# Kernel optimization log

Measured on AMD Instinct MI355X. Metric: run time of the kernel, lower is better.

The kernel has to match this reference:

```python
import jax, jax.numpy as jnp
import numpy as np

EPS = 1e-6
NUM_HEADS = 12


def _layernorm(x, eps=EPS):
    m = jnp.mean(x, axis=-1, keepdims=True)
    v = jnp.var(x, axis=-1, keepdims=True)
    return (x - m) * jax.lax.rsqrt(v + eps)


def _rmsnorm(x, w, eps=EPS):
    ms = jnp.mean(jnp.square(x), axis=-1, keepdims=True)
    return x * jax.lax.rsqrt(ms + eps) * w


def _rope_interleaved(x, cos, sin):
    # x: [B, L, H, hd]; cos/sin: [L, hd//2]; is_neox_style=False (interleaved pairs)
    x1 = x[..., 0::2]
    x2 = x[..., 1::2]
    c = cos[None, :, None, :]
    s = sin[None, :, None, :]
    o1 = x1 * c - x2 * s
    o2 = x1 * s + x2 * c
    return jnp.stack([o1, o2], axis=-1).reshape(x.shape)


def _attention(q, k, v, mask=None):
    # q: [B, Lq, H, hd], k/v: [B, Lk, H, hd]
    hd = q.shape[-1]
    scale = 1.0 / jnp.sqrt(jnp.asarray(hd, q.dtype))
    scores = jnp.einsum('blhd,bmhd->bhlm', q, k) * scale
    if mask is not None:
        scores = jnp.where(mask[None, None], scores, jnp.finfo(scores.dtype).min)
    p = jax.nn.softmax(scores, axis=-1)
    return jnp.einsum('bhlm,bmhd->blhd', p, v)


def setup_inputs() -> dict:
    key = jax.random.key(0)
    B, F, FS, D, FF, LC = 1, 2, 1560, 1536, 8960, 512
    L = F * FS
    hd = D // NUM_HEADS
    ks = jax.random.split(key, 32)
    i = iter(range(32))
    n = lambda shape, s=0.02: jax.random.normal(ks[next(i)], shape, jnp.float32) * s
    inp = {
        'hidden_states': n((B, L, D), 1.0),
        'encoder_hidden_states': n((B, LC, D), 1.0),
        'temb': n((B, F, 6, D), 1.0),
    }
    pos = jnp.arange(L, dtype=jnp.float32)
    inv = 1.0 / (10000.0 ** (jnp.arange(hd // 2, dtype=jnp.float32) / (hd // 2)))
    ang = pos[:, None] * inv[None, :]
    inp['cos'] = jnp.cos(ang)
    inp['sin'] = jnp.sin(ang)
    fidx = jnp.arange(L) // FS
    inp['attn_mask'] = fidx[:, None] >= fidx[None, :]  # frame-level block-causal
    # params
    inp['sst'] = n((1, 6, D), 1.0 / np.sqrt(D))
    for name in ['wq', 'wk', 'wv', 'wo']:
        inp[name] = n((D, D))
    for name in ['bq', 'bk', 'bv', 'bo']:
        inp[name] = jnp.zeros((D,), jnp.float32)
    inp['nq_w'] = jnp.ones((D,), jnp.float32)
    inp['nk_w'] = jnp.ones((D,), jnp.float32)
    inp['ln2_g'] = jnp.ones((D,), jnp.float32)
    inp['ln2_b'] = jnp.zeros((D,), jnp.float32)
    for name in ['cwq', 'cwk', 'cwv', 'cwo']:
        inp[name] = n((D, D))
    for name in ['cbq', 'cbk', 'cbv', 'cbo']:
        inp[name] = jnp.zeros((D,), jnp.float32)
    inp['cnq_w'] = jnp.ones((D,), jnp.float32)
    inp['cnk_w'] = jnp.ones((D,), jnp.float32)
    inp['w1'] = n((D, FF))
    inp['b1'] = jnp.zeros((FF,), jnp.float32)
    inp['w2'] = n((FF, D))
    inp['b2'] = jnp.zeros((D,), jnp.float32)
    return inp


def reference(hidden_states, encoder_hidden_states, temb, cos, sin, attn_mask,
              sst, wq, bq, wk, bk, wv, bv, wo, bo, nq_w, nk_w, ln2_g, ln2_b,
              cwq, cbq, cwk, cbk, cwv, cbv, cwo, cbo, cnq_w, cnk_w,
              w1, b1, w2, b2):
    B, L, D = hidden_states.shape
    F = temb.shape[1]
    FS = L // F
    H = NUM_HEADS
    hd = D // H

    e = sst[:, None] + temb  # [B, F, 6, D]
    shift_msa, scale_msa, gate_msa = e[:, :, 0], e[:, :, 1], e[:, :, 2]
    c_shift, c_scale, c_gate = e[:, :, 3], e[:, :, 4], e[:, :, 5]

    # --- self attention ---
    nh = _layernorm(hidden_states).reshape(B, F, FS, D)
    nh = (nh * (1.0 + scale_msa[:, :, None]) + shift_msa[:, :, None]).reshape(B, L, D)
    q = _rmsnorm(nh @ wq + bq, nq_w).reshape(B, L, H, hd)
    k = _rmsnorm(nh @ wk + bk, nk_w).reshape(B, L, H, hd)
    v = (nh @ wv + bv).reshape(B, L, H, hd)
    q = _rope_interleaved(q, cos, sin)
    k = _rope_interleaved(k, cos, sin)
    attn_out = _attention(q, k, v, attn_mask).reshape(B, L, D) @ wo + bo

    h = hidden_states + (attn_out.reshape(B, F, FS, D) * gate_msa[:, :, None]).reshape(B, L, D)
    norm_h = _layernorm(h) * ln2_g + ln2_b  # null shift/scale

    # --- cross attention ---
    LC = encoder_hidden_states.shape[1]
    cq = _rmsnorm(norm_h @ cwq + cbq, cnq_w).reshape(B, L, H, hd)
    ck = _rmsnorm(encoder_hidden_states @ cwk + cbk, cnk_w).reshape(B, LC, H, hd)
    cv = (encoder_hidden_states @ cwv + cbv).reshape(B, LC, H, hd)
    cross_out = _attention(cq, ck, cv).reshape(B, L, D) @ cwo + cbo

    h = h + cross_out  # gate = 1
    norm_h = _layernorm(h).reshape(B, F, FS, D)
    norm_h = (norm_h * (1.0 + c_scale[:, :, None]) + c_shift[:, :, None]).reshape(B, L, D)

    # --- ffn ---
    ff = jax.nn.gelu(norm_h @ w1 + b1, approximate=True) @ w2 + b2
    h = h + (ff.reshape(B, F, FS, D) * c_gate[:, :, None]).reshape(B, L, D)
    return h
```

## Files before the change

kernel.cpp:

```cpp
#include <hip/hip_runtime.h>
#include <hip/hip_bf16.h>
#include <math.h>

typedef __bf16 bf16;
typedef __bf16 bf16x8 __attribute__((ext_vector_type(8)));
typedef float  f32x4  __attribute__((ext_vector_type(4)));
typedef unsigned int u32;

#define DMODEL 1536
#define NHEADS 12
#define HD 128
#define HDH 64

__device__ __forceinline__ void async16(const void* g, void* l) {
  __builtin_amdgcn_global_load_lds((const __attribute__((address_space(1))) u32*)g,
                                   (__attribute__((address_space(3))) u32*)l, 16, 0, 0);
}

__device__ inline void block_reduce2(float& a, float& b) {
  __shared__ float sa[4], sb[4];
  #pragma unroll
  for (int off = 32; off; off >>= 1) {
    a += __shfl_xor(a, off);
    b += __shfl_xor(b, off);
  }
  int w = threadIdx.x >> 6;
  if ((threadIdx.x & 63) == 0) { sa[w] = a; sb[w] = b; }
  __syncthreads();
  a = sa[0] + sa[1] + sa[2] + sa[3];
  b = sb[0] + sb[1] + sb[2] + sb[3];
  __syncthreads();
}

__global__ __launch_bounds__(256)
void ln_kernel(const float* __restrict__ X, bf16* __restrict__ Y,
               const float* __restrict__ sst, const float* __restrict__ temb,
               const float* __restrict__ g, const float* __restrict__ bvec,
               int jshift, int jscale, int FS, int mode)
{
  int row = blockIdx.x;
  const float* x = X + (size_t)row * DMODEL;
  float v[6];
  float s1 = 0.f, s2 = 0.f;
  #pragma unroll
  for (int i = 0; i < 6; i++) {
    float t = x[threadIdx.x + i * 256];
    v[i] = t; s1 += t; s2 += t * t;
  }
  block_reduce2(s1, s2);
  float mean = s1 * (1.f / DMODEL);
  float var  = s2 * (1.f / DMODEL) - mean * mean;
  float rs = rsqrtf(var + 1e-6f);
  int f = row / FS;
  bf16* y = Y + (size_t)row * DMODEL;
  #pragma unroll
  for (int i = 0; i < 6; i++) {
    int d = threadIdx.x + i * 256;
    float t = (v[i] - mean) * rs;
    float o;
    if (mode == 0) {
      float sc = sst[jscale * DMODEL + d] + temb[(f * 6 + jscale) * DMODEL + d];
      float sh = sst[jshift * DMODEL + d] + temb[(f * 6 + jshift) * DMODEL + d];
      o = t * (1.f + sc) + sh;
    } else {
      o = t * g[d] + bvec[d];
    }
    y[d] = (bf16)o;
  }
}

__global__ __launch_bounds__(256)
void rms_rope_kernel(const float* __restrict__ P, int S, long long MN,
                     const bf16* __restrict__ Xb, int RS, int CO,
                     const float* __restrict__ bias, bf16* __restrict__ Y,
                     const float* __restrict__ w,
                     const float* __restrict__ cosb, const float* __restrict__ sinb,
                     int dorope, float oscale)
{
  __shared__ float rowbuf[DMODEL];
  int row = blockIdx.x;
  float v[6];
  float s2 = 0.f, dummy = 0.f;
  if (Xb) {
    const bf16* x = Xb + (size_t)row * RS + CO;
    #pragma unroll
    for (int i = 0; i < 6; i++) {
      int d = threadIdx.x + i * 256;
      float t = (float)x[d];
      v[i] = t; rowbuf[d] = t; s2 += t * t;
    }
  } else {
    const float* x = P + (size_t)row * RS + CO;
    #pragma unroll
    for (int i = 0; i < 6; i++) {
      int d = threadIdx.x + i * 256;
      float t = bias[d];
      for (int s = 0; s < S; s++) t += x[(size_t)s * MN + d];
      v[i] = t; rowbuf[d] = t; s2 += t * t;
    }
  }
  __syncthreads();
  block_reduce2(s2, dummy);
  float rs = rsqrtf(s2 * (1.f / DMODEL) + 1e-6f) * oscale;
  bf16* y = Y + (size_t)row * DMODEL;
  if (dorope) {
    #pragma unroll
    for (int i = 0; i < 3; i++) {
      int p = threadIdx.x + i * 256;
      int d0 = 2 * p, d1 = 2 * p + 1;
      float y0 = rowbuf[d0] * rs * w[d0];
      float y1 = rowbuf[d1] * rs * w[d1];
      int ih = p & 63;
      float c = cosb[(size_t)row * HDH + ih];
      float s = sinb[(size_t)row * HDH + ih];
      y[d0] = (bf16)(y0 * c - y1 * s);
      y[d1] = (bf16)(y0 * s + y1 * c);
    }
  } else {
    #pragma unroll
    for (int i = 0; i < 6; i++) {
      int d = threadIdx.x + i * 256;
      y[d] = (bf16)(v[i] * rs * w[d]);
    }
  }
}

__global__ __launch_bounds__(256)
void wt_kernel(const float* __restrict__ W, bf16* __restrict__ Wt, int K, int N)
{
  __shared__ float T[32][33];
  int k0 = blockIdx.x * 32, n0 = blockIdx.y * 32;
  int tx = threadIdx.x & 31, ty = threadIdx.x >> 5;
  #pragma unroll
  for (int i = 0; i < 4; i++)
    T[ty + 8 * i][tx] = W[(size_t)(k0 + ty + 8 * i) * N + n0 + tx];
  __syncthreads();
  #pragma unroll
  for (int i = 0; i < 4; i++)
    Wt[(size_t)(n0 + ty + 8 * i) * K + k0 + tx] = (bf16)T[tx][ty + 8 * i];
}

__global__ __launch_bounds__(256)
void catbias_kernel(float* __restrict__ bqkv, const float* __restrict__ bq,
                    const float* __restrict__ bk, const float* __restrict__ bv,
                    float* __restrict__ cbkv, const float* __restrict__ cbk,
                    const float* __restrict__ cbv)
{
  int i = blockIdx.x * 256 + threadIdx.x;
  if (i < DMODEL) {
    bqkv[i] = bq[i]; bqkv[DMODEL + i] = bk[i]; bqkv[2 * DMODEL + i] = bv[i];
    cbkv[i] = cbk[i]; cbkv[DMODEL + i] = cbv[i];
  }
}

__global__ __launch_bounds__(256)
void gemm_bt(const bf16* __restrict__ A, const bf16* __restrict__ Bt,
             const float* __restrict__ bias, float* __restrict__ Cf,
             bf16* __restrict__ Cb, int M, int N, int K, int act,
             int Ks, long long MN)
{
  __shared__ bf16 As[128 * 32];
  __shared__ bf16 Bs[128 * 32];
  int tid = threadIdx.x, lane = tid & 63, w = tid >> 6;
  int wm = w >> 1, wn = w & 1;
  int l16 = lane & 15, quad = lane >> 4;

  int gx = (M + 127) >> 7, gy = N >> 7;
  int per_panel = gx << 3;
  int bid = blockIdx.x;
  int panel = bid / per_panel;
  int rem = bid - panel * per_panel;
  int pc0 = panel << 3;
  int ncols = gy - pc0; if (ncols > 8) ncols = 8;
  int by = pc0 + rem % ncols;
  int bx = rem / ncols;
  int bm = bx * 128, bn = by * 128;

  int kb0 = blockIdx.y * Ks;

  int rl = lane >> 2;
  int kk = (lane & 3) * 8;
  int r0 = (2 * w) * 16 + rl, r1 = (2 * w + 1) * 16 + rl;
  int am0 = bm + r0; if (am0 > M - 1) am0 = M - 1;
  int am1 = bm + r1; if (am1 > M - 1) am1 = M - 1;
  const bf16* a0 = A + (size_t)am0 * K + kk;
  const bf16* a1 = A + (size_t)am1 * K + kk;
  const bf16* b0 = Bt + (size_t)(bn + r0) * K + kk;
  const bf16* b1 = Bt + (size_t)(bn + r1) * K + kk;
  bf16* lA0 = As + (2 * w) * 512; bf16* lA1 = As + (2 * w + 1) * 512;
  bf16* lB0 = Bs + (2 * w) * 512; bf16* lB1 = Bs + (2 * w + 1) * 512;

  f32x4 acc[4][4] = {};
  int kend = kb0 + Ks;
  for (int k0 = kb0; k0 < kend; k0 += 32) {
    async16(a0 + k0, lA0);
    async16(a1 + k0, lA1);
    async16(b0 + k0, lB0);
    async16(b1 + k0, lB1);
    __syncthreads();
    bf16x8 af[4], bfv[4];
    #pragma unroll
    for (int mi = 0; mi < 4; mi++)
      af[mi] = *(const bf16x8*)&As[(wm * 64 + mi * 16 + l16) * 32 + quad * 8];
    #pragma unroll
    for (int ni = 0; ni < 4; ni++)
      bfv[ni] = *(const bf16x8*)&Bs[(wn * 64 + ni * 16 + l16) * 32 + quad * 8];
    #pragma unroll
    for (int mi = 0; mi < 4; mi++)
      #pragma unroll
      for (int ni = 0; ni < 4; ni++)
        acc[mi][ni] = __builtin_amdgcn_mfma_f32_16x16x32_bf16(af[mi], bfv[ni], acc[mi][ni], 0, 0, 0);
    __syncthreads();
  }
  float* Cfo = Cf ? Cf + (size_t)blockIdx.y * MN : nullptr;
  #pragma unroll
  for (int mi = 0; mi < 4; mi++) {
    #pragma unroll
    for (int r = 0; r < 4; r++) {
      int m = bm + wm * 64 + mi * 16 + quad * 4 + r;
      if (m < M) {
        #pragma unroll
        for (int ni = 0; ni < 4; ni++) {
          int n = bn + wn * 64 + ni * 16 + l16;
          float val = acc[mi][ni][r] + (bias ? bias[n] : 0.f);
          if (act == 1) {
            float u = val + 0.044715f * val * val * val;
            float z = 1.5957691216057308f * u;
            val = val / (1.f + __expf(-z));
          }
          if (Cfo) Cfo[(size_t)m * N + n] = val;
          else     Cb[(size_t)m * N + n] = (bf16)val;
        }
      }
    }
  }
}

__global__ __launch_bounds__(512, 2)
void gemm256(const bf16* __restrict__ A, const bf16* __restrict__ Bt,
             const float* __restrict__ bias, float* __restrict__ Cf,
             bf16* __restrict__ Cb, int M, int N, int K, int act,
             int Ks, long long MN)
{
  __shared__ bf16 LDS[2][2][128 * 128];
  int tid = threadIdx.x, lane = tid & 63, w = tid >> 6;
  int wm = w >> 2, wn = w & 3;
  int l16 = lane & 15, quad = lane >> 4;

  int gmx = (M + 255) >> 8;
  int bx = blockIdx.x % gmx, by = blockIdx.x / gmx;
  int bm = bx << 8, bn = by << 8;
  int kb0 = blockIdx.y * Ks;
  int NT = Ks >> 6;

  int aro = (l16 * 64 + quad * 16) ^ ((l16 >> 3) << 5);
  const char* A0r = (const char*)&LDS[0][0][0] + wm * 16384 + aro;
  const char* A1r = (const char*)&LDS[1][0][0] + wm * 16384 + aro;
  const char* B0r = (const char*)&LDS[0][1][0] + wn * 8192 + aro;
  const char* B1r = (const char*)&LDS[1][1][0] + wn * 8192 + aro;

  int srl = lane >> 2;
  int sc16 = (lane & 3) ^ (((lane >> 5) & 1) << 1);
  int Mm1 = M - 1, Nm1 = N - 1;
  int ga0 = bm + w * 16 + srl;        if (ga0 > Mm1) ga0 = Mm1;
  int ga1 = bm + 128 + w * 16 + srl;  if (ga1 > Mm1) ga1 = Mm1;
  int gb0 = bn + w * 16 + srl;        if (gb0 > Nm1) gb0 = Nm1;
  int gb1 = bn + 128 + w * 16 + srl;  if (gb1 > Nm1) gb1 = Nm1;
  const bf16* Ag0 = A + (size_t)ga0 * K + sc16 * 8;
  const bf16* Ag1 = A + (size_t)ga1 * K + sc16 * 8;
  const bf16* Bg0 = Bt + (size_t)gb0 * K + sc16 * 8;
  const bf16* Bg1 = Bt + (size_t)gb1 * K + sc16 * 8;
  char* wA0[2] = { (char*)&LDS[0][0][0] + w * 2048, (char*)&LDS[1][0][0] + w * 2048 };
  char* wA1[2] = { wA0[0] + 16384, wA0[1] + 16384 };
  char* wB0[2] = { (char*)&LDS[0][1][0] + w * 2048, (char*)&LDS[1][1][0] + w * 2048 };
  char* wB1[2] = { wB0[0] + 16384, wB0[1] + 16384 };

#define STG(src, kk_, dst) do { const bf16* _s = (src) + (kk_); \
    async16(_s, (dst)); async16(_s + 32, (dst) + 1024); } while (0)
#define MFMA_(d, a, b) d = __builtin_amdgcn_mfma_f32_16x16x32_bf16(a, b, d, 0, 0, 0)

  STG(Ag0, kb0, wA0[0]); STG(Ag1, kb0, wA1[0]);
  STG(Bg0, kb0, wB0[0]); STG(Bg1, kb0, wB1[0]);
  if (NT > 1) {
    STG(Bg0, kb0 + 64, wB0[1]); STG(Bg1, kb0 + 64, wB1[1]);
    asm volatile("s_waitcnt vmcnt(4)" ::: "memory");
  } else {
    asm volatile("s_waitcnt vmcnt(0)" ::: "memory");
  }
  __builtin_amdgcn_s_barrier();

  f32x4 acc[8][4] = {};
  for (int t = 0; t < NT; ++t) {
    int b = t & 1;
    const char* Ab = b ? A1r : A0r;
    const char* Bb = b ? B1r : B0r;
    int kt1 = kb0 + (t + 1) * 64;
    int kt2 = kt1 + 64;
    bool st1 = (t + 1) < NT, st2 = (t + 2) < NT;

    bf16x8 a0[8], b0v[4];
    #pragma unroll
    for (int i = 0; i < 8; i++) a0[i] = *(const bf16x8*)(Ab + i * 1024);
    #pragma unroll
    for (int i = 0; i < 4; i++) b0v[i] = *(const bf16x8*)(Bb + i * 1024);
    if (st1) STG(Ag0, kt1, wA0[b ^ 1]);
    __builtin_amdgcn_s_barrier();
    asm volatile("s_waitcnt lgkmcnt(0)" ::: "memory");
    __builtin_amdgcn_s_setprio(1);
    #pragma unroll
    for (int mi = 0; mi < 4; mi++)
      #pragma unroll
      for (int ni = 0; ni < 2; ni++) {
        MFMA_(acc[mi][ni], a0[mi * 2],     b0v[ni * 2]);
        MFMA_(acc[mi][ni], a0[mi * 2 + 1], b0v[ni * 2 + 1]);
      }
    __builtin_amdgcn_s_setprio(0);
    __builtin_amdgcn_s_barrier();

    bf16x8 b1v[4];
    #pragma unroll
    for (int i = 0; i < 4; i++) b1v[i] = *(const bf16x8*)(Bb + (4 + i) * 1024);
    if (st1) STG(Ag1, kt1, wA1[b ^ 1]);
    __builtin_amdgcn_s_barrier();
    asm volatile("s_waitcnt lgkmcnt(0)" ::: "memory");
    __builtin_amdgcn_s_setprio(1);
    #pragma unroll
    for (int mi = 0; mi < 4; mi++)
      #pragma unroll
      for (int ni = 0; ni < 2; ni++) {
        MFMA_(acc[mi][2 + ni], a0[mi * 2],     b1v[ni * 2]);
        MFMA_(acc[mi][2 + ni], a0[mi * 2 + 1], b1v[ni * 2 + 1]);
      }
    __builtin_amdgcn_s_setprio(0);
    __builtin_amdgcn_s_barrier();

    bf16x8 a1[8];
    #pragma unroll
    for (int i = 0; i < 8; i++) a1[i] = *(const bf16x8*)(Ab + (8 + i) * 1024);
    if (st2) STG(Bg0, kt2, wB0[b]);
    __builtin_amdgcn_s_barrier();
    asm volatile("s_waitcnt lgkmcnt(0)" ::: "memory");
    __builtin_amdgcn_s_setprio(1);
    #pragma unroll
    for (int mi = 0; mi < 4; mi++)
      #pragma unroll
      for (int ni = 0; ni < 2; ni++) {
        MFMA_(acc[4 + mi][2 + ni], a1[mi * 2],     b1v[ni * 2]);
        MFMA_(acc[4 + mi][2 + ni], a1[mi * 2 + 1], b1v[ni * 2 + 1]);
      }
    __builtin_amdgcn_s_setprio(0);
    __builtin_amdgcn_s_barrier();

    if (st2) STG(Bg1, kt2, wB1[b]);
    __builtin_amdgcn_s_setprio(1);
    #pragma unroll
    for (int mi = 0; mi < 4; mi++)
      #pragma unroll
      for (int ni = 0; ni < 2; ni++) {
        MFMA_(acc[4 + mi][ni], a1[mi * 2],     b0v[ni * 2]);
        MFMA_(acc[4 + mi][ni], a1[mi * 2 + 1], b0v[ni * 2 + 1]);
      }
    __builtin_amdgcn_s_setprio(0);
    if (st2)      { asm volatile("s_waitcnt vmcnt(4)" ::: "memory"); }
    else if (st1) { asm volatile("s_waitcnt vmcnt(0)" ::: "memory"); }
    __builtin_amdgcn_s_barrier();
  }
#undef STG
#undef MFMA_

  float* Cfo = Cf ? Cf + (size_t)blockIdx.y * MN : nullptr;
  #pragma unroll
  for (int mi = 0; mi < 8; mi++) {
    #pragma unroll
    for (int r = 0; r < 4; r++) {
      int m = bm + wm * 128 + mi * 16 + quad * 4 + r;
      if (m < M) {
        #pragma unroll
        for (int ni = 0; ni < 4; ni++) {
          int n = bn + wn * 64 + ni * 16 + l16;
          float val = acc[mi][ni][r] + (bias ? bias[n] : 0.f);
          if (act == 1) {
            float u = val + 0.044715f * val * val * val;
            float z = 1.5957691216057308f * u;
            val = val / (1.f + __expf(-z));
          }
          if (Cfo) Cfo[(size_t)m * N + n] = val;
          else     Cb[(size_t)m * N + n] = (bf16)val;
        }
      }
    }
  }
}

__global__ __launch_bounds__(256)
void transposev_kernel(const bf16* __restrict__ Xb, int RS, int CO,
                       bf16* __restrict__ Vt, int L)
{
  __shared__ bf16 T[64][65];
  int l0 = blockIdx.x * 64, n0 = blockIdx.y * 64;
  int tid = threadIdx.x;
  int r = tid >> 2;
  int c8 = (tid & 3) * 16;
  int lc = l0 + r; if (lc > L - 1) lc = L - 1;
  const bf16* src = Xb + (size_t)lc * RS + CO + n0 + c8;
  #pragma unroll
  for (int i = 0; i < 16; i++) T[r][c8 + i] = src[i];
  __syncthreads();
  #pragma unroll
  for (int i = 0; i < 16; i++) {
    int l = l0 + c8 + i;
    if (l < L) Vt[(size_t)(n0 + r) * L + l] = T[c8 + i][r];
  }
}

__global__ __launch_bounds__(256)
void flash2_kernel(const bf16* __restrict__ Q, const bf16* __restrict__ Kg,
                   const bf16* __restrict__ Vt, bf16* __restrict__ O,
                   int Lq, int Lk, int FS, int causal, int nqb)
{
  __shared__ bf16 Kt[64 * 128];
  __shared__ bf16 Vtile[128 * 64];
  __shared__ bf16 Pl[4][16][72];
  int tid = threadIdx.x, lane = tid & 63, w = tid >> 6;
  int l16 = lane & 15, quad = lane >> 4;
  int bid = blockIdx.x;
  int h = bid % NHEADS;
  int qb = nqb - 1 - (bid / NHEADS);
  int q0b = qb * 64;
  int q0w = q0b + w * 16;

  int qrow = q0w + l16; if (qrow > Lq - 1) qrow = Lq - 1;
  const bf16* qbase = Q + (size_t)qrow * DMODEL + h * HD + quad * 8;
  bf16x8 qf[4];
  #pragma unroll
  for (int dc = 0; dc < 4; dc++) qf[dc] = *(const bf16x8*)(qbase + dc * 32);

  int kvrow[4];
  int kvmin_w = Lk, kv_end = Lk;
  if (causal) {
    #pragma unroll
    for (int r = 0; r < 4; r++) {
      int qr = q0w + quad * 4 + r; if (qr > Lq - 1) qr = Lq - 1;
      kvrow[r] = (qr / FS + 1) * FS;
    }
    int q0c = q0w; if (q0c > Lq - 1) q0c = Lq - 1;
    kvmin_w = (q0c / FS + 1) * FS;
    int qlast = q0b + 63; if (qlast > Lq - 1) qlast = Lq - 1;
    kv_end = (qlast / FS + 1) * FS;
    if (kv_end > Lk) kv_end = Lk;
  }

  f32x4 acc_o[8] = {};
  float m_i[4], l_i[4];
  #pragma unroll
  for (int r = 0; r < 4; r++) { m_i[r] = -1e30f; l_i[r] = 0.f; }

  for (int kb = 0; kb < kv_end; kb += 64) {
    #pragma unroll
    for (int j = 0; j < 4; j++) {
      int u = w * 256 + j * 64 + lane;
      int row = u >> 4;
      int c = (u & 15) ^ (row & 15);
      int krow = kb + row; if (krow > Lk - 1) krow = Lk - 1;
      async16(Kg + (size_t)krow * DMODEL + h * HD + c * 8,
              Kt + (size_t)(w * 256 + j * 64) * 8);
    }
    #pragma unroll
    for (int j = 0; j < 4; j++) {
      int u = w * 256 + j * 64 + lane;
      int row = u >> 3;
      int c = (u & 7) ^ (row & 7);
      async16(Vt + (size_t)(h * HD + row) * Lk + kb + c * 8,
              Vtile + (size_t)(w * 256 + j * 64) * 8);
    }
    __syncthreads();

    f32x4 s[4] = {};
    #pragma unroll
    for (int nk = 0; nk < 4; nk++) {
      #pragma unroll
      for (int dc = 0; dc < 4; dc++) {
        bf16x8 kf = *(const bf16x8*)&Kt[(((nk * 16 + l16) << 4) + ((4 * dc + quad) ^ l16)) * 8];
        s[nk] = __builtin_amdgcn_mfma_f32_16x16x32_bf16(qf[dc], kf, s[nk], 0, 0, 0);
      }
    }

    bool need_mask = causal && (kb + 64 > kvmin_w);
    float p[4][4];
    #pragma unroll
    for (int r = 0; r < 4; r++) {
      #pragma unroll
      for (int nk = 0; nk < 4; nk++) {
        float sv = s[nk][r];
        if (need_mask && (kb + nk * 16 + l16 >= kvrow[r])) sv = -1e30f;
        p[nk][r] = sv;
      }
      float bm = fmaxf(fmaxf(p[0][r], p[1][r]), fmaxf(p[2][r], p[3][r]));
      #pragma unroll
      for (int off = 8; off; off >>= 1) bm = fmaxf(bm, __shfl_xor(bm, off));
      float mn = fmaxf(m_i[r], bm);
      float alpha = __expf(m_i[r] - mn);
      m_i[r] = mn;
      float ps = 0.f;
      #pragma unroll
      for (int nk = 0; nk < 4; nk++) {
        float e = __expf(p[nk][r] - mn);
        p[nk][r] = e; ps += e;
      }
      #pragma unroll
      for (int off = 8; off; off >>= 1) ps += __shfl_xor(ps, off);
      l_i[r] = l_i[r] * alpha + ps;
      #pragma unroll
      for (int t = 0; t < 8; t++) acc_o[t][r] *= alpha;
    }

    #pragma unroll
    for (int nk = 0; nk < 4; nk++)
      #pragma unroll
      for (int r = 0; r < 4; r++)
        Pl[w][quad * 4 + r][nk * 16 + l16] = (bf16)p[nk][r];
    __threadfence_block();
    bf16x8 pf0 = *(const bf16x8*)&Pl[w][l16][quad * 8];
    bf16x8 pf1 = *(const bf16x8*)&Pl[w][l16][32 + quad * 8];

    #pragma unroll
    for (int t = 0; t < 8; t++) {
      bf16x8 vf0 = *(const bf16x8*)&Vtile[(((t * 16 + l16) << 3) + ((quad) ^ (l16 & 7))) * 8];
      bf16x8 vf1 = *(const bf16x8*)&Vtile[(((t * 16 + l16) << 3) + ((4 + quad) ^ (l16 & 7))) * 8];
      acc_o[t] = __builtin_amdgcn_mfma_f32_16x16x32_bf16(pf0, vf0, acc_o[t], 0, 0, 0);
      acc_o[t] = __builtin_amdgcn_mfma_f32_16x16x32_bf16(pf1, vf1, acc_o[t], 0, 0, 0);
    }
    __syncthreads();
  }

  #pragma unroll
  for (int r = 0; r < 4; r++) {
    int m = q0w + quad * 4 + r;
    if (m < Lq) {
      float inv = 1.f / l_i[r];
      bf16* obase = O + (size_t)m * DMODEL + h * HD;
      #pragma unroll
      for (int t = 0; t < 8; t++)
        obase[t * 16 + l16] = (bf16)(acc_o[t][r] * inv);
    }
  }
}

__global__ __launch_bounds__(256)
void modresid_kernel(const float* __restrict__ base, const float* __restrict__ P,
                     int S, long long MN, const float* __restrict__ bias,
                     float* __restrict__ out,
                     const float* __restrict__ sst, const float* __restrict__ temb,
                     int jg, int FS, long long total)
{
  long long i = (long long)blockIdx.x * 256 + threadIdx.x;
  if (i >= total) return;
  int d = (int)(i % DMODEL);
  int f = (int)((i / DMODEL) / FS);
  float g = sst[jg * DMODEL + d] + temb[(f * 6 + jg) * DMODEL + d];
  float v = bias[d];
  for (int s = 0; s < S; s++) v += P[(size_t)s * MN + i];
  out[i] = base[i] + v * g;
}

__global__ __launch_bounds__(256)
void addf_kernel(float* __restrict__ h, const float* __restrict__ P,
                 int S, long long MN, const float* __restrict__ bias, long long total)
{
  long long i = (long long)blockIdx.x * 256 + threadIdx.x;
  if (i >= total) return;
  int d = (int)(i % DMODEL);
  float v = bias[d];
  for (int s = 0; s < S; s++) v += P[(size_t)s * MN + i];
  h[i] += v;
}

__global__ __launch_bounds__(256)
void cast_kernel(const float* __restrict__ x, bf16* __restrict__ y, long long total)
{
  long long i = (long long)blockIdx.x * 256 + threadIdx.x;
  if (i < total) y[i] = (bf16)x[i];
}

extern "C" void kernel_launch(void* const* d_in, const int* in_sizes, int n_in,
                              void* d_out, int out_size, void* d_ws, size_t ws_size,
                              hipStream_t stream)
{
  const float* hs   = (const float*)d_in[0];
  const float* enc  = (const float*)d_in[1];
  const float* temb = (const float*)d_in[2];
  const float* cosb = (const float*)d_in[3];
  const float* sinb = (const float*)d_in[4];
  const float* sst  = (const float*)d_in[6];
  const float* wq = (const float*)d_in[7];
  const float* wk = (const float*)d_in[8];
  const float* wv = (const float*)d_in[9];
  const float* wo = (const float*)d_in[10];
  const float* bq = (const float*)d_in[11];
  const float* bk = (const float*)d_in[12];
  const float* bv = (const float*)d_in[13];
  const float* bo = (const float*)d_in[14];
  const float* nq_w = (const float*)d_in[15];
  const float* nk_w = (const float*)d_in[16];
  const float* ln2_g = (const float*)d_in[17];
  const float* ln2_b = (const float*)d_in[18];
  const float* cwq = (const float*)d_in[19];
  const float* cwk = (const float*)d_in[20];
  const float* cwv = (const float*)d_in[21];
  const float* cwo = (const float*)d_in[22];
  const float* cbq = (const float*)d_in[23];
  const float* cbk = (const float*)d_in[24];
  const float* cbv = (const float*)d_in[25];
  const float* cbo = (const float*)d_in[26];
  const float* cnq_w = (const float*)d_in[27];
  const float* cnk_w = (const float*)d_in[28];
  const float* w1 = (const float*)d_in[29];
  const float* b1 = (const float*)d_in[30];
  const float* w2 = (const float*)d_in[31];
  const float* b2 = (const float*)d_in[32];

  int L  = in_sizes[0] / DMODEL;
  int LC = in_sizes[1] / DMODEL;
  int F  = in_sizes[2] / (6 * DMODEL);
  int FS = L / F;
  int FF = in_sizes[30];
  long long LD = (long long)L * DMODEL;
  float* outp = (float*)d_out;
  int N3 = 3 * DMODEL, N2 = 2 * DMODEL;

  char* p = (char*)d_ws;
  auto alloc = [&](size_t bytes) -> char* {
    char* r = p; p += (bytes + 255) & ~(size_t)255; return r;
  };
  size_t DD = (size_t)DMODEL * DMODEL;
  bf16* wqkv_t = (bf16*)alloc(DD * 3 * 2);
  bf16* wto_t  = (bf16*)alloc(DD * 2);
  bf16* cwq_t  = (bf16*)alloc(DD * 2);
  bf16* cwkv_t = (bf16*)alloc(DD * 2 * 2);
  bf16* cwo_t  = (bf16*)alloc(DD * 2);
  bf16* w1t = (bf16*)alloc((size_t)DMODEL * FF * 2);
  bf16* w2t = (bf16*)alloc((size_t)DMODEL * FF * 2);
  float* bqkv = (float*)alloc((size_t)N3 * 4);
  float* cbkv = (float*)alloc((size_t)N2 * 4);
  float* hbuf = (float*)alloc((size_t)LD * 4);
  bf16* nh   = (bf16*)alloc((size_t)LD * 2);
  bf16* qb   = (bf16*)alloc((size_t)LD * 2);
  bf16* kb   = (bf16*)alloc((size_t)LD * 2);
  bf16* ab   = (bf16*)alloc((size_t)LD * 2);
  bf16* vtc  = (bf16*)alloc((size_t)LC * DMODEL * 2);
  bf16* encb = (bf16*)alloc((size_t)LC * DMODEL * 2);
  char* BIG1 = alloc((size_t)L * FF * 2);
  bf16* qkvb = (bf16*)BIG1;
  bf16* ckvb = (bf16*)BIG1;
  bf16* ffb  = (bf16*)BIG1;
  char* BIG2 = alloc((size_t)LD * 2 * 4);
  bf16* vtb = (bf16*)BIG2;
  float* Pp = (float*)BIG2;
  (void)ws_size; (void)n_in; (void)out_size;

  dim3 gWdd(DMODEL / 32, DMODEL / 32);
  wt_kernel<<<gWdd, 256, 0, stream>>>(wq, wqkv_t, DMODEL, DMODEL);
  wt_kernel<<<gWdd, 256, 0, stream>>>(wk, wqkv_t + DD, DMODEL, DMODEL);
  wt_kernel<<<gWdd, 256, 0, stream>>>(wv, wqkv_t + 2 * DD, DMODEL, DMODEL);
  wt_kernel<<<gWdd, 256, 0, stream>>>(wo, wto_t, DMODEL, DMODEL);
  wt_kernel<<<gWdd, 256, 0, stream>>>(cwq, cwq_t, DMODEL, DMODEL);
  wt_kernel<<<gWdd, 256, 0, stream>>>(cwk, cwkv_t, DMODEL, DMODEL);
  wt_kernel<<<gWdd, 256, 0, stream>>>(cwv, cwkv_t + DD, DMODEL, DMODEL);
  wt_kernel<<<gWdd, 256, 0, stream>>>(cwo, cwo_t, DMODEL, DMODEL);
  wt_kernel<<<dim3(DMODEL / 32, FF / 32), 256, 0, stream>>>(w1, w1t, DMODEL, FF);
  wt_kernel<<<dim3(FF / 32, DMODEL / 32), 256, 0, stream>>>(w2, w2t, FF, DMODEL);
  catbias_kernel<<<6, 256, 0, stream>>>(bqkv, bq, bk, bv, cbkv, cbk, cbv);

  int gxC = (LC + 127) / 128;
  int gmx = (L + 255) / 256;
  int ewg = (int)((LD + 255) / 256);
  int nqb = (L + 63) / 64;
  const float qs = 0.08838834764831845f;

  ln_kernel<<<L, 256, 0, stream>>>(hs, nh, sst, temb, nullptr, nullptr, 0, 1, FS, 0);
  gemm256<<<dim3(gmx * (N3 / 256), 1), 512, 0, stream>>>(nh, wqkv_t, bqkv, nullptr, qkvb,
                                                         L, N3, DMODEL, 0, DMODEL, 0);
  rms_rope_kernel<<<L, 256, 0, stream>>>(nullptr, 0, 0, qkvb, N3, 0, nullptr, qb, nq_w, cosb, sinb, 1, qs);
  rms_rope_kernel<<<L, 256, 0, stream>>>(nullptr, 0, 0, qkvb, N3, DMODEL, nullptr, kb, nk_w, cosb, sinb, 1, 1.0f);
  transposev_kernel<<<dim3((L + 63) / 64, DMODEL / 64), 256, 0, stream>>>(qkvb, N3, 2 * DMODEL, vtb, L);
  flash2_kernel<<<NHEADS * nqb, 256, 0, stream>>>(qb, kb, vtb, ab, L, L, FS, 1, nqb);
  gemm256<<<dim3(gmx * (DMODEL / 256), 2), 512, 0, stream>>>(ab, wto_t, nullptr, Pp, nullptr,
                                                             L, DMODEL, DMODEL, 0, DMODEL / 2, LD);
  modresid_kernel<<<ewg, 256, 0, stream>>>(hs, Pp, 2, LD, bo, hbuf, sst, temb, 2, FS, LD);
  ln_kernel<<<L, 256, 0, stream>>>(hbuf, nh, nullptr, nullptr, ln2_g, ln2_b, 0, 0, FS, 1);
  gemm256<<<dim3(gmx * (DMODEL / 256), 2), 512, 0, stream>>>(nh, cwq_t, nullptr, Pp, nullptr,
                                                             L, DMODEL, DMODEL, 0, DMODEL / 2, LD);
  rms_rope_kernel<<<L, 256, 0, stream>>>(Pp, 2, LD, nullptr, DMODEL, 0, cbq, qb, cnq_w, nullptr, nullptr, 0, qs);
  cast_kernel<<<(int)(((long long)LC * DMODEL + 255) / 256), 256, 0, stream>>>(enc, encb, (long long)LC * DMODEL);
  gemm_bt<<<dim3(gxC * (N2 / 128), 1), 256, 0, stream>>>(encb, cwkv_t, cbkv, nullptr, ckvb,
                                                         LC, N2, DMODEL, 0, DMODEL, 0);
  rms_rope_kernel<<<LC, 256, 0, stream>>>(nullptr, 0, 0, ckvb, N2, 0, nullptr, kb, cnk_w, nullptr, nullptr, 0, 1.0f);
  transposev_kernel<<<dim3((LC + 63) / 64, DMODEL / 64), 256, 0, stream>>>(ckvb, N2, DMODEL, vtc, LC);
  flash2_kernel<<<NHEADS * nqb, 256, 0, stream>>>(qb, kb, vtc, ab, L, LC, FS, 0, nqb);
  gemm256<<<dim3(gmx * (DMODEL / 256), 2), 512, 0, stream>>>(ab, cwo_t, nullptr, Pp, nullptr,
                                                             L, DMODEL, DMODEL, 0, DMODEL / 2, LD);
  addf_kernel<<<ewg, 256, 0, stream>>>(hbuf, Pp, 2, LD, cbo, LD);
  ln_kernel<<<L, 256, 0, stream>>>(hbuf, nh, sst, temb, nullptr, nullptr, 3, 4, FS, 0);
  gemm256<<<dim3(gmx * (FF / 256), 1), 512, 0, stream>>>(nh, w1t, b1, nullptr, ffb,
                                                         L, FF, DMODEL, 1, DMODEL, 0);
  gemm256<<<dim3(gmx * (DMODEL / 256), 2), 512, 0, stream>>>(ffb, w2t, nullptr, Pp, nullptr,
                                                             L, DMODEL, FF, 0, FF / 2, LD);
  modresid_kernel<<<ewg, 256, 0, stream>>>(hbuf, Pp, 2, LD, b2, outp, sst, temb, 5, FS, LD);
}
```

Baseline: 1.157 ms.

## Use grouped panel tile ordering and three-way uneven split-K in GEMMs

Tile indices in gemm256 now follow a panel order: runs of up to eight N-tiles are walked across all M-tiles, so concurrent blocks share B columns for better L2 reuse. Split-K now takes a split count and divides the 64-wide K tiles unevenly, allowing three splits even when K/64 does not divide evenly. The DMODEL-output GEMMs move from 2 to 3 splits to fill more CUs on a 12x6 tile grid. The cost is more fp32 partial-sum traffic and a larger workspace, which the reduction kernels now read as three partials.

```diff
diff --git a/kernel.cpp b/kernel.cpp
--- a/kernel.cpp
+++ b/kernel.cpp
@@ -240,18 +240,30 @@
 void gemm256(const bf16* __restrict__ A, const bf16* __restrict__ Bt,
              const float* __restrict__ bias, float* __restrict__ Cf,
              bf16* __restrict__ Cb, int M, int N, int K, int act,
-             int Ks, long long MN)
+             int S, long long MN)
 {
   __shared__ bf16 LDS[2][2][128 * 128];
   int tid = threadIdx.x, lane = tid & 63, w = tid >> 6;
   int wm = w >> 2, wn = w & 3;
   int l16 = lane & 15, quad = lane >> 4;
 
-  int gmx = (M + 255) >> 8;
-  int bx = blockIdx.x % gmx, by = blockIdx.x / gmx;
+  int gmx = (M + 255) >> 8, gny = N >> 8;
+  int per_panel = gmx << 3;
+  int bid = blockIdx.x;
+  int panel = bid / per_panel;
+  int rem = bid - panel * per_panel;
+  int pc0 = panel << 3;
+  int ncols = gny - pc0; if (ncols > 8) ncols = 8;
+  int by = pc0 + rem % ncols;
+  int bx = rem / ncols;
   int bm = bx << 8, bn = by << 8;
-  int kb0 = blockIdx.y * Ks;
-  int NT = Ks >> 6;
+
+  int NTtot = K >> 6;
+  int sidx = blockIdx.y;
+  int basek = NTtot / S, remk = NTtot % S;
+  int NT = basek + (sidx < remk ? 1 : 0);
+  int t0k = sidx * basek + (sidx < remk ? sidx : remk);
+  int kb0 = t0k << 6;
 
   int aro = (l16 * 64 + quad * 16) ^ ((l16 >> 3) << 5);
   const char* A0r = (const char*)&LDS[0][0][0] + wm * 16384 + aro;
@@ -653,7 +665,7 @@
   bf16* qkvb = (bf16*)BIG1;
   bf16* ckvb = (bf16*)BIG1;
   bf16* ffb  = (bf16*)BIG1;
-  char* BIG2 = alloc((size_t)LD * 2 * 4);
+  char* BIG2 = alloc((size_t)LD * 3 * 4);
   bf16* vtb = (bf16*)BIG2;
   float* Pp = (float*)BIG2;
   (void)ws_size; (void)n_in; (void)out_size;
@@ -679,31 +691,31 @@
 
   ln_kernel<<<L, 256, 0, stream>>>(hs, nh, sst, temb, nullptr, nullptr, 0, 1, FS, 0);
   gemm256<<<dim3(gmx * (N3 / 256), 1), 512, 0, stream>>>(nh, wqkv_t, bqkv, nullptr, qkvb,
-                                                         L, N3, DMODEL, 0, DMODEL, 0);
+                                                         L, N3, DMODEL, 0, 1, 0);
   rms_rope_kernel<<<L, 256, 0, stream>>>(nullptr, 0, 0, qkvb, N3, 0, nullptr, qb, nq_w, cosb, sinb, 1, qs);
   rms_rope_kernel<<<L, 256, 0, stream>>>(nullptr, 0, 0, qkvb, N3, DMODEL, nullptr, kb, nk_w, cosb, sinb, 1, 1.0f);
   transposev_kernel<<<dim3((L + 63) / 64, DMODEL / 64), 256, 0, stream>>>(qkvb, N3, 2 * DMODEL, vtb, L);
   flash2_kernel<<<NHEADS * nqb, 256, 0, stream>>>(qb, kb, vtb, ab, L, L, FS, 1, nqb);
-  gemm256<<<dim3(gmx * (DMODEL / 256), 2), 512, 0, stream>>>(ab, wto_t, nullptr, Pp, nullptr,
-                                                             L, DMODEL, DMODEL, 0, DMODEL / 2, LD);
-  modresid_kernel<<<ewg, 256, 0, stream>>>(hs, Pp, 2, LD, bo, hbuf, sst, temb, 2, FS, LD);
+  gemm256<<<dim3(gmx * (DMODEL / 256), 3), 512, 0, stream>>>(ab, wto_t, nullptr, Pp, nullptr,
+                                                             L, DMODEL, DMODEL, 0, 3, LD);
+  modresid_kernel<<<ewg, 256, 0, stream>>>(hs, Pp, 3, LD, bo, hbuf, sst, temb, 2, FS, LD);
   ln_kernel<<<L, 256, 0, stream>>>(hbuf, nh, nullptr, nullptr, ln2_g, ln2_b, 0, 0, FS, 1);
-  gemm256<<<dim3(gmx * (DMODEL / 256), 2), 512, 0, stream>>>(nh, cwq_t, nullptr, Pp, nullptr,
-                                                             L, DMODEL, DMODEL, 0, DMODEL / 2, LD);
-  rms_rope_kernel<<<L, 256, 0, stream>>>(Pp, 2, LD, nullptr, DMODEL, 0, cbq, qb, cnq_w, nullptr, nullptr, 0, qs);
+  gemm256<<<dim3(gmx * (DMODEL / 256), 3), 512, 0, stream>>>(nh, cwq_t, nullptr, Pp, nullptr,
+                                                             L, DMODEL, DMODEL, 0, 3, LD);
+  rms_rope_kernel<<<L, 256, 0, stream>>>(Pp, 3, LD, nullptr, DMODEL, 0, cbq, qb, cnq_w, nullptr, nullptr, 0, qs);
   cast_kernel<<<(int)(((long long)LC * DMODEL + 255) / 256), 256, 0, stream>>>(enc, encb, (long long)LC * DMODEL);
   gemm_bt<<<dim3(gxC * (N2 / 128), 1), 256, 0, stream>>>(encb, cwkv_t, cbkv, nullptr, ckvb,
                                                          LC, N2, DMODEL, 0, DMODEL, 0);
   rms_rope_kernel<<<LC, 256, 0, stream>>>(nullptr, 0, 0, ckvb, N2, 0, nullptr, kb, cnk_w, nullptr, nullptr, 0, 1.0f);
   transposev_kernel<<<dim3((LC + 63) / 64, DMODEL / 64), 256, 0, stream>>>(ckvb, N2, DMODEL, vtc, LC);
   flash2_kernel<<<NHEADS * nqb, 256, 0, stream>>>(qb, kb, vtc, ab, L, LC, FS, 0, nqb);
-  gemm256<<<dim3(gmx * (DMODEL / 256), 2), 512, 0, stream>>>(ab, cwo_t, nullptr, Pp, nullptr,
-                                                             L, DMODEL, DMODEL, 0, DMODEL / 2, LD);
-  addf_kernel<<<ewg, 256, 0, stream>>>(hbuf, Pp, 2, LD, cbo, LD);
+  gemm256<<<dim3(gmx * (DMODEL / 256), 3), 512, 0, stream>>>(ab, cwo_t, nullptr, Pp, nullptr,
+                                                             L, DMODEL, DMODEL, 0, 3, LD);
+  addf_kernel<<<ewg, 256, 0, stream>>>(hbuf, Pp, 3, LD, cbo, LD);
   ln_kernel<<<L, 256, 0, stream>>>(hbuf, nh, sst, temb, nullptr, nullptr, 3, 4, FS, 0);
   gemm256<<<dim3(gmx * (FF / 256), 1), 512, 0, stream>>>(nh, w1t, b1, nullptr, ffb,
-                                                         L, FF, DMODEL, 1, DMODEL, 0);
-  gemm256<<<dim3(gmx * (DMODEL / 256), 2), 512, 0, stream>>>(ffb, w2t, nullptr, Pp, nullptr,
-                                                             L, DMODEL, FF, 0, FF / 2, LD);
-  modresid_kernel<<<ewg, 256, 0, stream>>>(hbuf, Pp, 2, LD, b2, outp, sst, temb, 5, FS, LD);
-}
+                                                         L, FF, DMODEL, 1, 1, 0);
+  gemm256<<<dim3(gmx * (DMODEL / 256), 3), 512, 0, stream>>>(ffb, w2t, nullptr, Pp, nullptr,
+                                                             L, DMODEL, FF, 0, 3, LD);
+  modresid_kernel<<<ewg, 256, 0, stream>>>(hbuf, Pp, 3, LD, b2, outp, sst, temb, 5, FS, LD);
+}
```

After: 1.113 ms. -3.9%, faster.
